# Performance work log

Measured on AMD Instinct MI355X. Metric: run time of the kernel, lower is better.

The kernel has to match this reference:

```python
import jax, jax.numpy as jnp
import numpy as np
from jax import lax

COCO_80_TO_91 = [1,2,3,4,5,6,7,8,9,10,11,13,14,15,16,17,18,19,20,21,22,23,24,25,27,28,31,32,33,34,35,36,37,38,39,40,41,42,43,44,46,47,48,49,50,51,52,53,54,55,56,57,58,59,60,61,62,63,64,65,67,70,72,73,74,75,76,77,78,79,80,81,82,84,85,86,87,88,89,90]

CONF = 0.25      # self.confidence
IOU_THR = 0.7    # ultralytics NMS default
TOPK = 1000      # candidate cap before NMS
MAX_DET = 300    # ultralytics max_det default
MAX_WH = 7680.0  # per-class offset trick
IMG_SZ = 640.0   # yolov8 letterboxed input size


def setup_inputs() -> dict:
    key = jax.random.key(0)
    preds = jax.random.uniform(key, (32, 84, 8400), dtype=jnp.float32)
    return {"preds": preds}


def _nms_single(boxes, scores):
    """Greedy NMS on score-descending boxes [K,4] (class-offset xyxy). Returns keep mask [K]."""
    K = boxes.shape[0]
    area = (boxes[:, 2] - boxes[:, 0]) * (boxes[:, 3] - boxes[:, 1])  # [K]
    lt = jnp.maximum(boxes[:, None, :2], boxes[None, :, :2])          # [K,K,2]
    rb = jnp.minimum(boxes[:, None, 2:], boxes[None, :, 2:])
    wh = jnp.clip(rb - lt, 0.0)
    inter = wh[..., 0] * wh[..., 1]
    iou = inter / (area[:, None] + area[None, :] - inter + 1e-7)       # [K,K]
    idx = jnp.arange(K)
    sup = (iou > IOU_THR) & (idx[None, :] > idx[:, None])              # i suppresses later j

    def body(i, keep):
        return jnp.where(keep[i], keep & ~sup[i], keep)

    return lax.fori_loop(0, K, body, jnp.ones((K,), dtype=bool))


def reference(preds):
    # preds: [B, 84, N] -> [B, N, 84]
    p = jnp.transpose(preds, (0, 2, 1))
    box_xywh = p[..., :4] * IMG_SZ           # xywh in pixels on 640x640 canvas
    cls = p[..., 4:]                          # [B, N, 80]
    scores = jnp.max(cls, axis=-1)            # best-class confidence
    labels = jnp.argmax(cls, axis=-1)         # 0..79
    xy, wh = box_xywh[..., :2], box_xywh[..., 2:]
    xyxy = jnp.concatenate([xy - wh * 0.5, xy + wh * 0.5], axis=-1)  # decode

    # confidence filter + top-K candidate selection (score-descending)
    s_masked = jnp.where(scores > CONF, scores, -1.0)
    top_s, top_i = lax.top_k(s_masked, TOPK)                          # [B,TOPK]
    top_b = jnp.take_along_axis(xyxy, top_i[..., None], axis=1)      # [B,TOPK,4]
    top_l = jnp.take_along_axis(labels, top_i, axis=1)               # [B,TOPK]

    # per-class NMS via class offset
    off_b = top_b + (top_l.astype(top_b.dtype) * MAX_WH)[..., None]
    keep = jax.vmap(_nms_single)(off_b, top_s) & (top_s > CONF)

    # select final max_det detections, zero-pad invalid slots
    fin_s = jnp.where(keep, top_s, -1.0)
    out_s, out_i = lax.top_k(fin_s, MAX_DET)                          # [B,MAX_DET]
    out_b = jnp.take_along_axis(top_b, out_i[..., None], axis=1)
    out_l = jnp.take_along_axis(top_l, out_i, axis=1)
    valid = out_s > CONF
    boxes = jnp.where(valid[..., None], out_b, 0.0)
    scores_out = jnp.where(valid, out_s, 0.0)
    mapped = jnp.asarray(COCO_80_TO_91, dtype=jnp.int64)[out_l]       # COCO 80 -> 91 ids
    labels_out = jnp.where(valid, mapped, 0)
    return boxes, scores_out, labels_out
```

## Files before the change

kernel.cpp:

```cpp
#include <hip/hip_runtime.h>
#include <stdint.h>

typedef unsigned long long u64;
typedef unsigned int u32;

#define BATCH 32
#define NCH 84
#define NA 8400
#define NCLS 80
#define TOPK 1000
#define MAXDET 300
#define CONF 0.25f
#define IOU_T 0.7f
#define MAX_WH 7680.0f
#define IMG_SZ 640.0f
#define NT 1024
#define KPT 9
#define NCOPY 8
#define HPAD 260

__device__ __constant__ float coco_map_f[NCLS] = {
    1,2,3,4,5,6,7,8,9,10,11,13,14,15,16,17,18,19,20,21,22,23,24,25,27,28,
    31,32,33,34,35,36,37,38,39,40,41,42,43,44,46,47,48,49,50,51,52,53,54,
    55,56,57,58,59,60,61,62,63,64,65,67,70,72,73,74,75,76,77,78,79,80,81,
    82,84,85,86,87,88,89,90};

__device__ inline u64 shflx64(u64 v, int m) {
    int lo = __shfl_xor((int)(u32)(v & 0xFFFFFFFFull), m, 64);
    int hi = __shfl_xor((int)(u32)(v >> 32), m, 64);
    return ((u64)(u32)hi << 32) | (u32)lo;
}

__global__ __launch_bounds__(256)
void decode_kernel(const float* __restrict__ preds,
                   u64* __restrict__ keys,
                   float4* __restrict__ boxes,
                   int* __restrict__ labels) {
    const int QPB = NA / 4;
    int gid = blockIdx.x * 256 + threadIdx.x;
    if (gid >= BATCH * QPB) return;
    int b = gid / QPB;
    int q = gid - b * QPB;
    int a0 = q * 4;
    const float* p = preds + (size_t)b * NCH * NA + a0;

    float4 x = *(const float4*)(p);
    float4 y = *(const float4*)(p + NA);
    float4 w = *(const float4*)(p + 2 * NA);
    float4 h = *(const float4*)(p + 3 * NA);

    float4 best = *(const float4*)(p + 4 * NA);
    int lx = 0, ly = 0, lz = 0, lw = 0;
#pragma unroll 16
    for (int c = 1; c < NCLS; ++c) {
        const float4 v = *(const float4*)(p + (size_t)(4 + c) * NA);
        lx = (v.x > best.x) ? c : lx;  best.x = fmaxf(v.x, best.x);
        ly = (v.y > best.y) ? c : ly;  best.y = fmaxf(v.y, best.y);
        lz = (v.z > best.z) ? c : lz;  best.z = fmaxf(v.z, best.z);
        lw = (v.w > best.w) ? c : lw;  best.w = fmaxf(v.w, best.w);
    }

    float bs[4] = {best.x, best.y, best.z, best.w};
    int   bl[4] = {lx, ly, lz, lw};
    float cx[4] = {x.x, x.y, x.z, x.w};
    float cy[4] = {y.x, y.y, y.z, y.w};
    float cw[4] = {w.x, w.y, w.z, w.w};
    float ch[4] = {h.x, h.y, h.z, h.w};

    u64* kp = keys + (size_t)b * NA + a0;
    float4* bp = boxes + (size_t)b * NA + a0;
    int* lp = labels + (size_t)b * NA + a0;

#pragma unroll
    for (int i = 0; i < 4; ++i) {
        float fx = cx[i] * IMG_SZ, fy = cy[i] * IMG_SZ;
        float fw = cw[i] * IMG_SZ, fh = ch[i] * IMG_SZ;
        float hw = fw * 0.5f, hh = fh * 0.5f;
        bp[i] = make_float4(fx - hw, fy - hh, fx + hw, fy + hh);
        float s = (bs[i] > CONF) ? bs[i] : -1.0f;
        u32 fb = __float_as_uint(s);
        u32 u = (fb & 0x80000000u) ? ~fb : (fb | 0x80000000u);
        kp[i] = ((u64)u << 14) | (u64)(16383 - (a0 + i));
    }
    *(int4*)lp = make_int4(bl[0], bl[1], bl[2], bl[3]);
}

__global__ __launch_bounds__(NT)
void topk_sort_kernel(const u64* __restrict__ keys,
                      u64* __restrict__ sorted) {
    const int b = blockIdx.x;
    const int t = threadIdx.x;
    const int lane = t & 63, wid = t >> 6;

    __shared__ u64 sk[2][NT];
    __shared__ int sh_hist[NCOPY * HPAD];
    __shared__ int selB, selK, hselS, smax, scnt, cnt;

    u64 kreg[KPT];
    const u64* kb = keys + (size_t)b * NA;
    int nk = 0;
    for (int i = t; i < NA; i += NT) kreg[nk++] = kb[i];

    u64 P = 0ull;
    int kk = TOPK;
    int nsel = 0;
    for (int d = 5; d >= 0; --d) {
        __syncthreads();
        if (t == 0) { smax = -1; scnt = 0; }
        __syncthreads();
        u64 hmask = (~0ull) << (8 * (d + 1));
        int dig[KPT];
        int mymax = -1;
#pragma unroll
        for (int i = 0; i < KPT; ++i) {
            bool act = (i < nk) && (((kreg[i] ^ P) & hmask) == 0ull);
            dig[i] = act ? (int)((kreg[i] >> (8 * d)) & 255) : -1;
            mymax = max(mymax, dig[i]);
        }
#pragma unroll
        for (int off = 32; off; off >>= 1)
            mymax = max(mymax, __shfl_down(mymax, off, 64));
        if (lane == 0) atomicMax(&smax, mymax);
        __syncthreads();
        int maxb = smax;
        int myc = 0;
#pragma unroll
        for (int i = 0; i < KPT; ++i) myc += (dig[i] == maxb) ? 1 : 0;
#pragma unroll
        for (int off = 32; off; off >>= 1) myc += __shfl_down(myc, off, 64);
        if (lane == 0) atomicAdd(&scnt, myc);
        __syncthreads();
        int cm = scnt;
        if (cm >= kk) {
            P |= ((u64)maxb) << (8 * d);
            nsel = TOPK - kk + cm;
            if (nsel <= NT) break;
            continue;
        }
        for (int i = t; i < NCOPY * HPAD; i += NT) sh_hist[i] = 0;
        __syncthreads();
        int* myh = sh_hist + (wid & (NCOPY - 1)) * HPAD;
#pragma unroll
        for (int i = 0; i < KPT; ++i)
            if (dig[i] >= 0) atomicAdd(&myh[dig[i]], 1);
        __syncthreads();
        if (t < 64) {
            int h0 = 0, h1 = 0, h2 = 0, h3 = 0;
            for (int c = 0; c < NCOPY; ++c) {
                const int* hp = sh_hist + c * HPAD + 4 * t;
                h0 += hp[0]; h1 += hp[1]; h2 += hp[2]; h3 += hp[3];
            }
            int s = h0 + h1 + h2 + h3;
            int S = s;
            #pragma unroll
            for (int off = 1; off < 64; off <<= 1) {
                int o = __shfl_down(S, off, 64);
                if (t + off < 64) S += o;
            }
            int Snext = S - s;
            int c3 = Snext + h3, c2 = c3 + h2, c1 = c2 + h1, c0 = c1 + h0;
            int cand = -1, above = 0;
            if (c0 >= kk) {
                if      (c3 >= kk) { cand = 4 * t + 3; above = Snext; }
                else if (c2 >= kk) { cand = 4 * t + 2; above = c3; }
                else if (c1 >= kk) { cand = 4 * t + 1; above = c2; }
                else               { cand = 4 * t;     above = c1; }
            }
            int pc = (cand < 0) ? 0 : (((cand + 1) << 16) | (kk - above));
            #pragma unroll
            for (int off = 32; off; off >>= 1)
                pc = max(pc, __shfl_down(pc, off, 64));
            pc = __shfl(pc, 0, 64);
            int B = (pc >> 16) - 1;
            if (t == (B >> 2)) {
                int m4 = B & 3;
                selB = B;
                selK = pc & 0xFFFF;
                hselS = (m4 == 0) ? h0 : (m4 == 1) ? h1 : (m4 == 2) ? h2 : h3;
            }
        }
        __syncthreads();
        P |= ((u64)selB) << (8 * d);
        kk = selK;
        nsel = TOPK - kk + hselS;
        if (nsel <= NT) break;
    }

    __syncthreads();
    if (t == 0) cnt = 0;
    __syncthreads();
    for (int i = 0; i < KPT; ++i) {
        bool p = (i < nk) && (kreg[i] >= P);
        u64 m = __ballot(p);
        int base = 0;
        if (lane == 0) base = atomicAdd(&cnt, (int)__popcll(m));
        base = __shfl(base, 0, 64);
        if (p) sk[0][base + (int)__popcll(m & ((1ull << lane) - 1ull))] = kreg[i];
    }
    if (t < NT - nsel) sk[0][nsel + t] = 0ull;
    __syncthreads();

    u64 myk = sk[0][t];
    int buf = 1;
    for (int size = 2; size <= NT; size <<= 1) {
        bool up = ((t & size) == 0);
        for (int stride = size >> 1; stride; stride >>= 1) {
            u64 pk;
            if (stride >= 64) {
                sk[buf][t] = myk;
                __syncthreads();
                pk = sk[buf][t ^ stride];
                buf ^= 1;
            } else {
                pk = shflx64(myk, stride);
            }
            bool tlow = ((t & stride) == 0);
            u64 mn = (myk < pk) ? myk : pk;
            u64 mx = (myk < pk) ? pk : myk;
            myk = up ? (tlow ? mx : mn) : (tlow ? mn : mx);
        }
    }
    sorted[(size_t)b * NT + t] = myk;
}

__global__ __launch_bounds__(NT)
void nms_kernel(const u64* __restrict__ sorted,
                const float4* __restrict__ boxes,
                const int* __restrict__ labels,
                float* __restrict__ out) {
    const int b = blockIdx.x;
    const int t = threadIdx.x;
    const int lane = t & 63, wid = t >> 6;

    __shared__ float offb[TOPK][4];
    __shared__ float area_s[TOPK];
    __shared__ unsigned char lb8[TOPK];
    __shared__ unsigned char keep[TOPK];
    __shared__ u64 cmask2[NCLS][16];
    __shared__ unsigned short rows[NCLS][64];
    __shared__ int ktot_s;
    __shared__ int wsum[16], woff[16];

    u64 myk = sorted[(size_t)b * NT + t];

    for (int i = t; i < NCLS * 16; i += NT) ((u64*)cmask2)[i] = 0ull;
    __syncthreads();

    int my_a = -1, my_L = 0;
    if (t < TOPK) {
        my_a = 16383 - (int)(myk & 16383ull);
        my_L = labels[(size_t)b * NA + my_a];
        lb8[t] = (unsigned char)my_L;
        float4 bx = boxes[(size_t)b * NA + my_a];
        float off = (float)my_L * MAX_WH;
        float ox0 = bx.x + off, oy0 = bx.y + off, ox1 = bx.z + off, oy1 = bx.w + off;
        offb[t][0] = ox0; offb[t][1] = oy0; offb[t][2] = ox1; offb[t][3] = oy1;
        area_s[t] = (ox1 - ox0) * (oy1 - oy0);
        keep[t] = 1;
        atomicOr(&cmask2[my_L][t >> 6], 1ull << (t & 63));
    }
    __syncthreads();

    for (int c = wid; c < NCLS; c += 16) {
        u64 w = (lane < 16) ? cmask2[c][lane] : 0ull;
        int cw = __popcll(w);
        int pre = cw;
        #pragma unroll
        for (int off = 1; off < 16; off <<= 1) {
            int o = __shfl_up(pre, off, 64);
            if (lane >= off) pre += o;
        }
        int n = __shfl(pre, 15, 64);
        pre -= cw;
        if (n == 0) continue;
        if (n <= 64) {
            if (lane < 16) {
                u64 ww = w; int base = pre, boff = lane << 6;
                while (ww) {
                    int bit = __ffsll((long long)ww) - 1;
                    ww &= ww - 1;
                    rows[c][base++] = (unsigned short)(boff + bit);
                }
            }
            int j = (lane < n) ? (int)rows[c][lane] : (int)rows[c][0];
            float x0 = offb[j][0], y0 = offb[j][1];
            float x1 = offb[j][2], y1 = offb[j][3];
            float ar = area_s[j];
            u64 colm = 0ull;
            for (int i = 0; i < n; ++i) {
                float hx0 = __shfl(x0, i, 64);
                float hy0 = __shfl(y0, i, 64);
                float hx1 = __shfl(x1, i, 64);
                float hy1 = __shfl(y1, i, 64);
                float ha  = __shfl(ar, i, 64);
                float lx = fmaxf(hx0, x0), ly = fmaxf(hy0, y0);
                float rx = fminf(hx1, x1), ry = fminf(hy1, y1);
                float ww2 = fmaxf(rx - lx, 0.0f);
                float hh2 = fmaxf(ry - ly, 0.0f);
                float inter = ww2 * hh2;
                float denom = ha + ar;
                denom = denom - inter;
                denom = denom + 1e-7f;
                bool s = (lane > i) && (lane < n) && (inter / denom > IOU_T);
                colm |= ((u64)s) << i;
            }
            u64 alive = (n >= 64) ? ~0ull : ((1ull << n) - 1ull);
            for (int i = 0; i < n; ++i) {
                if (!((alive >> i) & 1ull)) continue;
                alive &= ~__ballot((colm >> i) & 1ull);
            }
            if (lane < n) keep[j] = (unsigned char)((alive >> lane) & 1ull);
        } else if (lane == 0) {
            for (int i = 0; i < TOPK; ++i) {
                if (lb8[i] != (unsigned char)c || !keep[i]) continue;
                float ax0 = offb[i][0], ay0 = offb[i][1];
                float ax1 = offb[i][2], ay1 = offb[i][3];
                float aa = area_s[i];
                for (int j2 = i + 1; j2 < TOPK; ++j2) {
                    if (lb8[j2] != (unsigned char)c || !keep[j2]) continue;
                    float lx = fmaxf(ax0, offb[j2][0]);
                    float ly = fmaxf(ay0, offb[j2][1]);
                    float rx = fminf(ax1, offb[j2][2]);
                    float ry = fminf(ay1, offb[j2][3]);
                    float ww2 = fmaxf(rx - lx, 0.0f);
                    float hh2 = fmaxf(ry - ly, 0.0f);
                    float inter = ww2 * hh2;
                    float denom = aa + area_s[j2];
                    denom = denom - inter;
                    denom = denom + 1e-7f;
                    if (inter / denom > IOU_T) keep[j2] = 0;
                }
            }
        }
    }
    __syncthreads();

    bool valid = false;
    float sj = 0.0f;
    if (t < TOPK) {
        u32 u = (u32)(myk >> 14);
        u32 fb = (u & 0x80000000u) ? (u ^ 0x80000000u) : ~u;
        sj = __uint_as_float(fb);
        valid = keep[t] && (sj > CONF);
    }
    u64 m = __ballot(valid);
    if (lane == 0) wsum[wid] = (int)__popcll(m);
    __syncthreads();
    if (wid == 0) {
        int v = (lane < 16) ? wsum[lane] : 0;
        #pragma unroll
        for (int off = 1; off < 16; off <<= 1) {
            int o = __shfl_up(v, off, 64);
            if (lane >= off) v += o;
        }
        if (lane < 16) woff[lane] = v - wsum[lane];
        if (lane == 15) ktot_s = v;
    }
    __syncthreads();
    int ktot = ktot_s;
    int rank = woff[wid] + (int)__popcll(m & ((1ull << lane) - 1ull));

    float* out_boxes = out;
    float* out_scores = out + (size_t)BATCH * MAXDET * 4;
    float* out_labels = out + (size_t)BATCH * MAXDET * 5;
    if (valid && rank < MAXDET) {
        float4 bx = boxes[(size_t)b * NA + my_a];
        float* ob = out_boxes + ((size_t)b * MAXDET + rank) * 4;
        ob[0] = bx.x; ob[1] = bx.y; ob[2] = bx.z; ob[3] = bx.w;
        out_scores[(size_t)b * MAXDET + rank] = sj;
        out_labels[(size_t)b * MAXDET + rank] = coco_map_f[my_L];
    }
    if (t < MAXDET && t >= ktot) {
        float* ob = out_boxes + ((size_t)b * MAXDET + t) * 4;
        ob[0] = 0.0f; ob[1] = 0.0f; ob[2] = 0.0f; ob[3] = 0.0f;
        out_scores[(size_t)b * MAXDET + t] = 0.0f;
        out_labels[(size_t)b * MAXDET + t] = 0.0f;
    }
}

extern "C" void kernel_launch(void* const* d_in, const int* in_sizes, int n_in,
                              void* d_out, int out_size, void* d_ws, size_t ws_size,
                              hipStream_t stream) {
    const float* preds = (const float*)d_in[0];
    char* ws = (char*)d_ws;

    const size_t keys_bytes   = (size_t)BATCH * NA * 8;
    const size_t boxes_bytes  = (size_t)BATCH * NA * 16;
    const size_t labels_bytes = (size_t)BATCH * NA * 4;

    u64* keys = (u64*)ws;
    float4* boxes = (float4*)(ws + keys_bytes);
    int* labels = (int*)(ws + keys_bytes + boxes_bytes);
    u64* sorted = (u64*)(ws + keys_bytes + boxes_bytes + labels_bytes);
    float* out = (float*)d_out;

    int total = BATCH * (NA / 4);
    decode_kernel<<<(total + 255) / 256, 256, 0, stream>>>(preds, keys, boxes, labels);
    topk_sort_kernel<<<BATCH, NT, 0, stream>>>(keys, sorted);
    nms_kernel<<<BATCH, NT, 0, stream>>>(sorted, boxes, labels, out);
}
```

Measured before the change: 187.8 us.

## Fuse top-k sort with NMS kernel and stage decode through shared memory

The top-k selection/bitonic sort kernel and the NMS kernel become one kernel, and their shared-memory buffers are overlaid through a union. This drops one launch and the global round trip of the sorted keys. The decode kernel is also restructured: each block tiles 256 anchors, stages 16 channel rows at a time into shared memory with float4 loads, and each thread then handles one anchor instead of four. The change trades fewer loads in flight per thread for coalesced tile loads, and adds extra barriers in decode.

```diff
diff --git a/kernel.cpp b/kernel.cpp
--- a/kernel.cpp
+++ b/kernel.cpp
@@ -18,6 +18,7 @@
 #define KPT 9
 #define NCOPY 8
 #define HPAD 260
+#define DTILE 256
 
 __device__ __constant__ float coco_map_f[NCLS] = {
     1,2,3,4,5,6,7,8,9,10,11,13,14,15,16,17,18,19,20,21,22,23,24,25,27,28,
@@ -36,65 +37,88 @@
                    u64* __restrict__ keys,
                    float4* __restrict__ boxes,
                    int* __restrict__ labels) {
-    const int QPB = NA / 4;
-    int gid = blockIdx.x * 256 + threadIdx.x;
-    if (gid >= BATCH * QPB) return;
-    int b = gid / QPB;
-    int q = gid - b * QPB;
-    int a0 = q * 4;
-    const float* p = preds + (size_t)b * NCH * NA + a0;
-
-    float4 x = *(const float4*)(p);
-    float4 y = *(const float4*)(p + NA);
-    float4 w = *(const float4*)(p + 2 * NA);
-    float4 h = *(const float4*)(p + 3 * NA);
-
-    float4 best = *(const float4*)(p + 4 * NA);
-    int lx = 0, ly = 0, lz = 0, lw = 0;
-#pragma unroll 16
-    for (int c = 1; c < NCLS; ++c) {
-        const float4 v = *(const float4*)(p + (size_t)(4 + c) * NA);
-        lx = (v.x > best.x) ? c : lx;  best.x = fmaxf(v.x, best.x);
-        ly = (v.y > best.y) ? c : ly;  best.y = fmaxf(v.y, best.y);
-        lz = (v.z > best.z) ? c : lz;  best.z = fmaxf(v.z, best.z);
-        lw = (v.w > best.w) ? c : lw;  best.w = fmaxf(v.w, best.w);
-    }
-
-    float bs[4] = {best.x, best.y, best.z, best.w};
-    int   bl[4] = {lx, ly, lz, lw};
-    float cx[4] = {x.x, x.y, x.z, x.w};
-    float cy[4] = {y.x, y.y, y.z, y.w};
-    float cw[4] = {w.x, w.y, w.z, w.w};
-    float ch[4] = {h.x, h.y, h.z, h.w};
-
-    u64* kp = keys + (size_t)b * NA + a0;
-    float4* bp = boxes + (size_t)b * NA + a0;
-    int* lp = labels + (size_t)b * NA + a0;
-
-#pragma unroll
-    for (int i = 0; i < 4; ++i) {
-        float fx = cx[i] * IMG_SZ, fy = cy[i] * IMG_SZ;
-        float fw = cw[i] * IMG_SZ, fh = ch[i] * IMG_SZ;
+    const int b = blockIdx.y;
+    const int a_base = blockIdx.x * DTILE;
+    const int t = threadIdx.x;
+    const int a = a_base + t;
+    const float* p = preds + (size_t)b * NCH * NA;
+
+    __shared__ float stage[16][DTILE];
+
+    float bx = 0.f, by = 0.f, bw = 0.f, bh = 0.f;
+    float best = -1.0f;
+    int bl = 0;
+
+    for (int chunk = 0; chunk < 6; ++chunk) {
+        const int r0 = chunk * 16;
+        const int nr = (chunk == 5) ? 4 : 16;
+        if (chunk) __syncthreads();
+        for (int i = 0; i < nr / 4; ++i) {
+            int idx = i * 256 + t;
+            int rl = idx >> 6;
+            int c4 = (idx & 63) * 4;
+            int col = a_base + c4;
+            float4 v = (col < NA) ? *(const float4*)(p + (size_t)(r0 + rl) * NA + col)
+                                  : make_float4(0.f, 0.f, 0.f, 0.f);
+            *(float4*)&stage[rl][c4] = v;
+        }
+        __syncthreads();
+        if (chunk == 0) {
+            bx = stage[0][t]; by = stage[1][t];
+            bw = stage[2][t]; bh = stage[3][t];
+            best = stage[4][t]; bl = 0;
+            for (int r = 5; r < 16; ++r) {
+                float v = stage[r][t];
+                int c = r - 4;
+                bl = (v > best) ? c : bl;  best = fmaxf(v, best);
+            }
+        } else {
+            for (int r = 0; r < nr; ++r) {
+                float v = stage[r][t];
+                int c = r0 + r - 4;
+                bl = (v > best) ? c : bl;  best = fmaxf(v, best);
+            }
+        }
+    }
+
+    if (a < NA) {
+        float fx = bx * IMG_SZ, fy = by * IMG_SZ;
+        float fw = bw * IMG_SZ, fh = bh * IMG_SZ;
         float hw = fw * 0.5f, hh = fh * 0.5f;
-        bp[i] = make_float4(fx - hw, fy - hh, fx + hw, fy + hh);
-        float s = (bs[i] > CONF) ? bs[i] : -1.0f;
+        boxes[(size_t)b * NA + a] = make_float4(fx - hw, fy - hh, fx + hw, fy + hh);
+        float s = (best > CONF) ? best : -1.0f;
         u32 fb = __float_as_uint(s);
         u32 u = (fb & 0x80000000u) ? ~fb : (fb | 0x80000000u);
-        kp[i] = ((u64)u << 14) | (u64)(16383 - (a0 + i));
-    }
-    *(int4*)lp = make_int4(bl[0], bl[1], bl[2], bl[3]);
+        keys[(size_t)b * NA + a] = ((u64)u << 14) | (u64)(16383 - a);
+        labels[(size_t)b * NA + a] = bl;
+    }
 }
 
 __global__ __launch_bounds__(NT)
-void topk_sort_kernel(const u64* __restrict__ keys,
-                      u64* __restrict__ sorted) {
+void select_nms_kernel(const u64* __restrict__ keys,
+                       const float4* __restrict__ boxes,
+                       const int* __restrict__ labels,
+                       float* __restrict__ out) {
     const int b = blockIdx.x;
     const int t = threadIdx.x;
     const int lane = t & 63, wid = t >> 6;
 
-    __shared__ u64 sk[2][NT];
-    __shared__ int sh_hist[NCOPY * HPAD];
-    __shared__ int selB, selK, hselS, smax, scnt, cnt;
+    __shared__ union {
+        struct {
+            u64 sk[2][NT];
+            int hist[NCOPY * HPAD];
+        } a;
+        struct {
+            float offb[TOPK][4];
+            float area[TOPK];
+            u64 cmask2[NCLS][16];
+            unsigned short rows[NCLS][64];
+        } bb;
+    } u_s;
+    __shared__ unsigned char lb8[TOPK];
+    __shared__ unsigned char keep[TOPK];
+    __shared__ int selB, selK, hselS, smax, scnt, cnt, ktot_s;
+    __shared__ int wsum[16], woff[16];
 
     u64 kreg[KPT];
     const u64* kb = keys + (size_t)b * NA;
@@ -137,9 +161,9 @@
             if (nsel <= NT) break;
             continue;
         }
-        for (int i = t; i < NCOPY * HPAD; i += NT) sh_hist[i] = 0;
-        __syncthreads();
-        int* myh = sh_hist + (wid & (NCOPY - 1)) * HPAD;
+        for (int i = t; i < NCOPY * HPAD; i += NT) u_s.a.hist[i] = 0;
+        __syncthreads();
+        int* myh = u_s.a.hist + (wid & (NCOPY - 1)) * HPAD;
 #pragma unroll
         for (int i = 0; i < KPT; ++i)
             if (dig[i] >= 0) atomicAdd(&myh[dig[i]], 1);
@@ -147,7 +171,7 @@
         if (t < 64) {
             int h0 = 0, h1 = 0, h2 = 0, h3 = 0;
             for (int c = 0; c < NCOPY; ++c) {
-                const int* hp = sh_hist + c * HPAD + 4 * t;
+                const int* hp = u_s.a.hist + c * HPAD + 4 * t;
                 h0 += hp[0]; h1 += hp[1]; h2 += hp[2]; h3 += hp[3];
             }
             int s = h0 + h1 + h2 + h3;
@@ -195,21 +219,21 @@
         int base = 0;
         if (lane == 0) base = atomicAdd(&cnt, (int)__popcll(m));
         base = __shfl(base, 0, 64);
-        if (p) sk[0][base + (int)__popcll(m & ((1ull << lane) - 1ull))] = kreg[i];
-    }
-    if (t < NT - nsel) sk[0][nsel + t] = 0ull;
-    __syncthreads();
-
-    u64 myk = sk[0][t];
+        if (p) u_s.a.sk[0][base + (int)__popcll(m & ((1ull << lane) - 1ull))] = kreg[i];
+    }
+    if (t < NT - nsel) u_s.a.sk[0][nsel + t] = 0ull;
+    __syncthreads();
+
+    u64 myk = u_s.a.sk[0][t];
     int buf = 1;
     for (int size = 2; size <= NT; size <<= 1) {
         bool up = ((t & size) == 0);
         for (int stride = size >> 1; stride; stride >>= 1) {
             u64 pk;
             if (stride >= 64) {
-                sk[buf][t] = myk;
+                u_s.a.sk[buf][t] = myk;
                 __syncthreads();
-                pk = sk[buf][t ^ stride];
+                pk = u_s.a.sk[buf][t ^ stride];
                 buf ^= 1;
             } else {
                 pk = shflx64(myk, stride);
@@ -220,30 +244,9 @@
             myk = up ? (tlow ? mx : mn) : (tlow ? mn : mx);
         }
     }
-    sorted[(size_t)b * NT + t] = myk;
-}
-
-__global__ __launch_bounds__(NT)
-void nms_kernel(const u64* __restrict__ sorted,
-                const float4* __restrict__ boxes,
-                const int* __restrict__ labels,
-                float* __restrict__ out) {
-    const int b = blockIdx.x;
-    const int t = threadIdx.x;
-    const int lane = t & 63, wid = t >> 6;
-
-    __shared__ float offb[TOPK][4];
-    __shared__ float area_s[TOPK];
-    __shared__ unsigned char lb8[TOPK];
-    __shared__ unsigned char keep[TOPK];
-    __shared__ u64 cmask2[NCLS][16];
-    __shared__ unsigned short rows[NCLS][64];
-    __shared__ int ktot_s;
-    __shared__ int wsum[16], woff[16];
-
-    u64 myk = sorted[(size_t)b * NT + t];
-
-    for (int i = t; i < NCLS * 16; i += NT) ((u64*)cmask2)[i] = 0ull;
+
+    __syncthreads();
+    for (int i = t; i < NCLS * 16; i += NT) ((u64*)u_s.bb.cmask2)[i] = 0ull;
     __syncthreads();
 
     int my_a = -1, my_L = 0;
@@ -254,15 +257,16 @@
         float4 bx = boxes[(size_t)b * NA + my_a];
         float off = (float)my_L * MAX_WH;
         float ox0 = bx.x + off, oy0 = bx.y + off, ox1 = bx.z + off, oy1 = bx.w + off;
-        offb[t][0] = ox0; offb[t][1] = oy0; offb[t][2] = ox1; offb[t][3] = oy1;
-        area_s[t] = (ox1 - ox0) * (oy1 - oy0);
+        u_s.bb.offb[t][0] = ox0; u_s.bb.offb[t][1] = oy0;
+        u_s.bb.offb[t][2] = ox1; u_s.bb.offb[t][3] = oy1;
+        u_s.bb.area[t] = (ox1 - ox0) * (oy1 - oy0);
         keep[t] = 1;
-        atomicOr(&cmask2[my_L][t >> 6], 1ull << (t & 63));
+        atomicOr(&u_s.bb.cmask2[my_L][t >> 6], 1ull << (t & 63));
     }
     __syncthreads();
 
     for (int c = wid; c < NCLS; c += 16) {
-        u64 w = (lane < 16) ? cmask2[c][lane] : 0ull;
+        u64 w = (lane < 16) ? u_s.bb.cmask2[c][lane] : 0ull;
         int cw = __popcll(w);
         int pre = cw;
         #pragma unroll
@@ -279,13 +283,13 @@
                 while (ww) {
                     int bit = __ffsll((long long)ww) - 1;
                     ww &= ww - 1;
-                    rows[c][base++] = (unsigned short)(boff + bit);
+                    u_s.bb.rows[c][base++] = (unsigned short)(boff + bit);
                 }
             }
-            int j = (lane < n) ? (int)rows[c][lane] : (int)rows[c][0];
-            float x0 = offb[j][0], y0 = offb[j][1];
-            float x1 = offb[j][2], y1 = offb[j][3];
-            float ar = area_s[j];
+            int j = (lane < n) ? (int)u_s.bb.rows[c][lane] : (int)u_s.bb.rows[c][0];
+            float x0 = u_s.bb.offb[j][0], y0 = u_s.bb.offb[j][1];
+            float x1 = u_s.bb.offb[j][2], y1 = u_s.bb.offb[j][3];
+            float ar = u_s.bb.area[j];
             u64 colm = 0ull;
             for (int i = 0; i < n; ++i) {
                 float hx0 = __shfl(x0, i, 64);
@@ -313,19 +317,19 @@
         } else if (lane == 0) {
             for (int i = 0; i < TOPK; ++i) {
                 if (lb8[i] != (unsigned char)c || !keep[i]) continue;
-                float ax0 = offb[i][0], ay0 = offb[i][1];
-                float ax1 = offb[i][2], ay1 = offb[i][3];
-                float aa = area_s[i];
+                float ax0 = u_s.bb.offb[i][0], ay0 = u_s.bb.offb[i][1];
+                float ax1 = u_s.bb.offb[i][2], ay1 = u_s.bb.offb[i][3];
+                float aa = u_s.bb.area[i];
                 for (int j2 = i + 1; j2 < TOPK; ++j2) {
                     if (lb8[j2] != (unsigned char)c || !keep[j2]) continue;
-                    float lx = fmaxf(ax0, offb[j2][0]);
-                    float ly = fmaxf(ay0, offb[j2][1]);
-                    float rx = fminf(ax1, offb[j2][2]);
-                    float ry = fminf(ay1, offb[j2][3]);
+                    float lx = fmaxf(ax0, u_s.bb.offb[j2][0]);
+                    float ly = fmaxf(ay0, u_s.bb.offb[j2][1]);
+                    float rx = fminf(ax1, u_s.bb.offb[j2][2]);
+                    float ry = fminf(ay1, u_s.bb.offb[j2][3]);
                     float ww2 = fmaxf(rx - lx, 0.0f);
                     float hh2 = fmaxf(ry - ly, 0.0f);
                     float inter = ww2 * hh2;
-                    float denom = aa + area_s[j2];
+                    float denom = aa + u_s.bb.area[j2];
                     denom = denom - inter;
                     denom = denom + 1e-7f;
                     if (inter / denom > IOU_T) keep[j2] = 0;
@@ -384,18 +388,15 @@
     const float* preds = (const float*)d_in[0];
     char* ws = (char*)d_ws;
 
-    const size_t keys_bytes   = (size_t)BATCH * NA * 8;
-    const size_t boxes_bytes  = (size_t)BATCH * NA * 16;
-    const size_t labels_bytes = (size_t)BATCH * NA * 4;
+    const size_t keys_bytes  = (size_t)BATCH * NA * 8;
+    const size_t boxes_bytes = (size_t)BATCH * NA * 16;
 
     u64* keys = (u64*)ws;
     float4* boxes = (float4*)(ws + keys_bytes);
     int* labels = (int*)(ws + keys_bytes + boxes_bytes);
-    u64* sorted = (u64*)(ws + keys_bytes + boxes_bytes + labels_bytes);
     float* out = (float*)d_out;
 
-    int total = BATCH * (NA / 4);
-    decode_kernel<<<(total + 255) / 256, 256, 0, stream>>>(preds, keys, boxes, labels);
-    topk_sort_kernel<<<BATCH, NT, 0, stream>>>(keys, sorted);
-    nms_kernel<<<BATCH, NT, 0, stream>>>(sorted, boxes, labels, out);
+    dim3 dgrid((NA + DTILE - 1) / DTILE, BATCH);
+    decode_kernel<<<dgrid, 256, 0, stream>>>(preds, keys, boxes, labels);
+    select_nms_kernel<<<BATCH, NT, 0, stream>>>(keys, boxes, labels, out);
 }
```

Measured after the change: 184.4 us. Within noise of the previous version (-1.8%).
